# Kernel tuning notes

Measured on AMD Instinct MI355X. Metric: run time of the kernel, lower is better.

Reference implementation:

```python
import jax, jax.numpy as jnp
import numpy as np

L = 24
D = 2048
NUM_BLOCKS = 8
EPS = 1e-6
B, T = 2, 1024


def _block_layout(num_layers, num_blocks):
    base = num_layers // num_blocks
    rem = num_layers % num_blocks
    sizes = [base] * num_blocks
    if rem:
        sizes[-1] += rem
    starts = list(np.cumsum([0] + sizes[:-1]))
    return sizes, starts


def _rmsnorm(x, weight, eps=EPS):
    # x: (..., d)
    var = jnp.mean(x * x, axis=-1, keepdims=True)
    return x * jax.lax.rsqrt(var + eps) * weight


def setup_inputs() -> dict:
    key = jax.random.key(0)
    k1, k2, k3 = jax.random.split(key, 3)
    layer_outputs = jax.random.normal(k1, (L, B, T, D), dtype=jnp.float32)
    embedding = jax.random.normal(k2, (B, T, D), dtype=jnp.float32)
    queries = jax.random.normal(k3, (L, D), dtype=jnp.float32) * 0.02
    key_norm_weight = jnp.ones((D,), dtype=jnp.float32)
    return {
        "layer_outputs": layer_outputs,
        "embedding": embedding,
        "queries": queries,
        "key_norm_weight": key_norm_weight,
    }


def reference(layer_outputs, embedding, queries, key_norm_weight):
    """Faithful port of BlockAttnRes.compute_all_inputs.

    layer_outputs: (L, B, T, d)  -- f_l(h_l) for each layer
    embedding:     (B, T, d)     -- b_0
    queries:       (L, d)        -- zero-init pseudo-queries (randn here)
    key_norm_weight: (d,)        -- RMSNorm scale
    Returns (L, B, T, d): AttnRes input h_l for each layer.
    """
    num_layers = layer_outputs.shape[0]
    sizes, starts = _block_layout(num_layers, NUM_BLOCKS)

    block_reprs = [embedding]
    partial = None
    inputs = []
    block_n = 0
    for l in range(num_layers):  # fixed structural loop over layers
        # advance block index
        while l >= starts[block_n] + sizes[block_n]:
            block_n += 1
        i = l - starts[block_n]
        sources = list(block_reprs)
        if i > 0 and partial is not None:
            sources.append(partial)
        v_stack = jnp.stack(sources, axis=2)            # (B, T, n, d)
        k_stack = _rmsnorm(v_stack, key_norm_weight)    # (B, T, n, d)
        scores = jnp.einsum("btnd,d->btn", k_stack, queries[l])
        alpha = jax.nn.softmax(scores, axis=-1)         # (B, T, n)
        h = jnp.einsum("btn,btnd->btd", alpha, v_stack)
        inputs.append(h)
        f_l = layer_outputs[l]
        partial = f_l if partial is None else partial + f_l
        if i + 1 >= sizes[block_n]:
            block_reprs.append(partial)
            partial = None
    return jnp.stack(inputs, axis=0)  # (L, B, T, d)
```

## Files before the change

### kernel.cpp

```cpp
#include <hip/hip_runtime.h>
#include <hip/hip_bf16.h>

constexpr int LAYERS = 24;
constexpr int DIM    = 2048;
constexpr int NBLK   = 8;
constexpr float EPSV = 1e-6f;
constexpr int TPB    = 512;
constexpr int EPT    = 4;
constexpr int NSLOT  = 147;
constexpr int RSTR   = NSLOT + 2;

typedef float vf4 __attribute__((ext_vector_type(4)));

__device__ constexpr int OFF_TAB[24] =
    {0,1,4,7,10,14,18,22,27,32,37,43,49,55,62,69,76,84,92,100,109,118,127,137};
__device__ constexpr int SSQS[7] = {9,21,36,54,75,99,126};

__device__ __forceinline__ unsigned pk2(float a, float b) {
    __hip_bfloat162 h2(__float2bfloat16(a), __float2bfloat16(b));
    union { __hip_bfloat162 h; unsigned u; } c; c.h = h2; return c.u;
}
__device__ __forceinline__ float upk(unsigned p, int hi) {
    union { unsigned u; float f; } c;
    c.u = hi ? (p & 0xffff0000u) : (p << 16);
    return c.f;
}

template<int CTRL>
__device__ __forceinline__ float dpp_add(float x) {
    int y = __builtin_amdgcn_update_dpp(0, __float_as_int(x), CTRL, 0xF, 0xF, true);
    return x + __int_as_float(y);
}
__device__ __forceinline__ float grp16_sum(float x) {
    x = dpp_add<0xB1>(x);
    x = dpp_add<0x4E>(x);
    x = dpp_add<0x141>(x);
    x = dpp_add<0x140>(x);
    return x;
}

__global__ void prep_qw_kernel(const float* __restrict__ q,
                               const float* __restrict__ w,
                               float* __restrict__ qw, int n) {
    int idx = blockIdx.x * blockDim.x + threadIdx.x;
    if (idx < n) qw[idx] = q[idx] * w[idx & (DIM - 1)];
}

template<bool PREMUL>
__global__ void __launch_bounds__(TPB, 4)
block_attn_res_kernel(const float* __restrict__ lo,
                      const float* __restrict__ emb,
                      const float* __restrict__ q1,
                      const float* __restrict__ wgt,
                      float* __restrict__ out,
                      int bt_total)
{
    const int bt   = blockIdx.x;
    const int tid  = threadIdx.x;
    const int lane = tid & 63;
    const int wid  = tid >> 6;
    const int grp  = (wid << 2) | (lane >> 4);
    const int c0   = tid * 4;

    __shared__ float red[32][RSTR];
    __shared__ float redJ[NSLOT + 1];
    __shared__ float ab[LAYERS][12];

    const float invD = 1.f / (float)DIM;
    const size_t lstride = (size_t)bt_total * DIM;
    const float* lop = lo + (size_t)bt * DIM + c0;

    auto wred = [&](float x, int slot) {
        x = grp16_sum(x);
        if ((lane & 15) == 0) red[grp][slot] = x;
    };

    float wv[EPT];
    if (!PREMUL) {
        vf4 w0 = *reinterpret_cast<const vf4*>(wgt + c0);
        wv[0]=w0.x; wv[1]=w0.y; wv[2]=w0.z; wv[3]=w0.w;
    }

    float e[EPT];
    {
        vf4 v0 = __builtin_nontemporal_load(
            reinterpret_cast<const vf4*>(emb + (size_t)bt * DIM + c0));
        e[0]=v0.x; e[1]=v0.y; e[2]=v0.z; e[3]=v0.w;
    }

    unsigned pp[16][EPT/2];
    unsigned Spk[NBLK-1][EPT/2];
    float part[EPT];

    {
        vf4 u0 = __builtin_nontemporal_load(reinterpret_cast<const vf4*>(lop));
        part[0]=u0.x; part[1]=u0.y; part[2]=u0.z; part[3]=u0.w;

        vf4 w0; w0.x=e[0]; w0.y=e[1]; w0.z=e[2]; w0.w=e[3];
        *reinterpret_cast<vf4*>(out + (size_t)bt * DIM + c0) = w0;

        float sq = e[0]*e[0] + e[1]*e[1] + e[2]*e[2] + e[3]*e[3];
        wred(sq, 0);
    }

    float fb[8][EPT], qb[2][EPT];
    {
        #pragma unroll
        for (int k = 1; k <= 8; ++k) {
            vf4 u = __builtin_nontemporal_load(
                reinterpret_cast<const vf4*>(lop + (size_t)k * lstride));
            fb[k & 7][0]=u.x; fb[k & 7][1]=u.y; fb[k & 7][2]=u.z; fb[k & 7][3]=u.w;
        }
        vf4 q;
        q = *reinterpret_cast<const vf4*>(q1 + (size_t)1 * DIM + c0);
        qb[1][0]=q.x; qb[1][1]=q.y; qb[1][2]=q.z; qb[1][3]=q.w;
        q = *reinterpret_cast<const vf4*>(q1 + (size_t)2 * DIM + c0);
        qb[0][0]=q.x; qb[0][1]=q.y; qb[0][2]=q.z; qb[0][3]=q.w;
    }

    #pragma unroll
    for (int l = 1; l < LAYERS; ++l) {
        const int m   = l / 3;
        const int i   = l - 3 * m;
        const int off = OFF_TAB[l];
        const int pf  = l & 7;
        const int pq  = l & 1;

        float qwv[EPT];
        #pragma unroll
        for (int j = 0; j < EPT; ++j)
            qwv[j] = PREMUL ? qb[pq][j] : qb[pq][j] * wv[j];
        float fC[EPT];
        if (l < LAYERS - 1) {
            #pragma unroll
            for (int j = 0; j < EPT; ++j) fC[j] = fb[pf][j];
        }

        if (l + 8 <= LAYERS - 2) {
            vf4 u0 = __builtin_nontemporal_load(
                reinterpret_cast<const vf4*>(lop + (size_t)(l + 8) * lstride));
            fb[pf][0]=u0.x; fb[pf][1]=u0.y; fb[pf][2]=u0.z; fb[pf][3]=u0.w;
        }
        if (l + 2 <= LAYERS - 1) {
            vf4 v0 = *reinterpret_cast<const vf4*>(q1 + (size_t)(l + 2) * DIM + c0);
            qb[pq][0]=v0.x; qb[pq][1]=v0.y; qb[pq][2]=v0.z; qb[pq][3]=v0.w;
        }

        {
            float dv = e[0]*qwv[0] + e[1]*qwv[1] + e[2]*qwv[2] + e[3]*qwv[3];
            wred(dv, off);
        }
        #pragma unroll
        for (int s = 0; s < NBLK - 1; ++s) {
            if (s < m) {
                float dv;
                if (s == m - 1 && i == 0) {
                    dv = part[0]*qwv[0] + part[1]*qwv[1]
                       + part[2]*qwv[2] + part[3]*qwv[3];
                } else {
                    dv = upk(Spk[s][0],0)*qwv[0] + upk(Spk[s][0],1)*qwv[1]
                       + upk(Spk[s][1],0)*qwv[2] + upk(Spk[s][1],1)*qwv[3];
                }
                wred(dv, off + 1 + s);
            }
        }
        if (i > 0) {
            float dv = part[0]*qwv[0] + part[1]*qwv[1]
                     + part[2]*qwv[2] + part[3]*qwv[3];
            float sq = part[0]*part[0] + part[1]*part[1]
                     + part[2]*part[2] + part[3]*part[3];
            wred(dv, off + m + 1);
            wred(sq, off + m + 2);
            const int si = 2 * m + (i - 1);
            pp[si][0] = pk2(part[0], part[1]);
            pp[si][1] = pk2(part[2], part[3]);
        } else {
            float sq = part[0]*part[0] + part[1]*part[1]
                     + part[2]*part[2] + part[3]*part[3];
            wred(sq, off + m + 1);
        }

        if (l < LAYERS - 1) {
            if (i == 0) {
                #pragma unroll
                for (int j = 0; j < EPT; ++j) part[j] = fC[j];
            } else {
                #pragma unroll
                for (int j = 0; j < EPT; ++j) part[j] += fC[j];
            }
            if (i == 2 && m < NBLK - 1) {
                Spk[m][0] = pk2(part[0], part[1]);
                Spk[m][1] = pk2(part[2], part[3]);
            }
        }
    }

    __syncthreads();

    if (tid < NSLOT) {
        float s = 0.f;
        #pragma unroll
        for (int g = 0; g < 32; ++g) s += red[g][tid];
        redJ[tid] = s;
    }
    __syncthreads();

    if (tid >= 1 && tid < LAYERS) {
        const int l = tid;
        const int m = l / 3;
        const int i = l - 3 * m;
        const int off = OFF_TAB[l];
        const float ssqe = redJ[0];
        float sce = redJ[off] * rsqrtf(ssqe * invD + EPSV);
        float mx = sce;
        float scS[NBLK - 1];
        #pragma unroll
        for (int s = 0; s < NBLK - 1; ++s) {
            if (s < m) {
                scS[s] = redJ[off + 1 + s] * rsqrtf(redJ[SSQS[s]] * invD + EPSV);
                mx = fmaxf(mx, scS[s]);
            }
        }
        float scp = 0.f;
        if (i > 0) {
            scp = redJ[off + m + 1] * rsqrtf(redJ[off + m + 2] * invD + EPSV);
            mx = fmaxf(mx, scp);
        }
        float ee = __expf(sce - mx), den = ee;
        float es[NBLK - 1];
        #pragma unroll
        for (int s = 0; s < NBLK - 1; ++s) {
            es[s] = (s < m) ? __expf(scS[s] - mx) : 0.f;
            den += es[s];
        }
        float ep = 0.f;
        if (i > 0) { ep = __expf(scp - mx); den += ep; }
        const float inv = 1.f / den;
        ab[l][0] = ee * inv;
        #pragma unroll
        for (int s = 0; s < NBLK - 1; ++s)
            if (s < m) ab[l][1 + s] = es[s] * inv;
        if (i > 0) ab[l][1 + m] = ep * inv;
    }
    __syncthreads();

    #pragma unroll
    for (int l = 1; l < LAYERS; ++l) {
        const int m = l / 3;
        const int i = l - 3 * m;

        float h[EPT];
        {
            const float a0 = ab[l][0];
            #pragma unroll
            for (int j = 0; j < EPT; ++j) h[j] = a0 * e[j];
        }
        #pragma unroll
        for (int s = 0; s < NBLK - 1; ++s) {
            if (s < m) {
                const float a = ab[l][1 + s];
                h[0] += a * upk(Spk[s][0],0);
                h[1] += a * upk(Spk[s][0],1);
                h[2] += a * upk(Spk[s][1],0);
                h[3] += a * upk(Spk[s][1],1);
            }
        }
        if (i > 0) {
            const float a = ab[l][1 + m];
            const int si = 2 * m + (i - 1);
            h[0] += a * upk(pp[si][0],0);
            h[1] += a * upk(pp[si][0],1);
            h[2] += a * upk(pp[si][1],0);
            h[3] += a * upk(pp[si][1],1);
        }

        {
            vf4 w0; w0.x=h[0]; w0.y=h[1]; w0.z=h[2]; w0.w=h[3];
            *reinterpret_cast<vf4*>(out + ((size_t)l * bt_total + bt) * DIM + c0) = w0;
        }
    }
}

extern "C" void kernel_launch(void* const* d_in, const int* in_sizes, int n_in,
                              void* d_out, int out_size, void* d_ws, size_t ws_size,
                              hipStream_t stream) {
    const float* lo  = (const float*)d_in[0];
    const float* emb = (const float*)d_in[1];
    const float* qry = (const float*)d_in[2];
    const float* wgt = (const float*)d_in[3];
    float* outp = (float*)d_out;

    const int bt_total = in_sizes[1] / DIM;
    const int nq = in_sizes[2];

    if (ws_size >= (size_t)nq * sizeof(float)) {
        float* qwbuf = (float*)d_ws;
        prep_qw_kernel<<<(nq + 255) / 256, 256, 0, stream>>>(qry, wgt, qwbuf, nq);
        block_attn_res_kernel<true><<<bt_total, TPB, 0, stream>>>(
            lo, emb, qwbuf, nullptr, outp, bt_total);
    } else {
        block_attn_res_kernel<false><<<bt_total, TPB, 0, stream>>>(
            lo, emb, qry, wgt, outp, bt_total);
    }
}
```

Before: 195.6 us.

## Split layer pipeline in two halves to overlap output writes with loads

Splits the per-row computation into two phases. After the first 11 layers, the partial reductions and softmax for those layers are computed. Their outputs are then emitted, interleaved with the score accumulation for layers 12-23, so stores overlap the remaining loads. The prefetch depth for layer outputs drops from 8 to 4 slots, which frees registers. The cost is extra block-wide barriers and a shallower load pipeline.

```diff
diff --git a/kernel.cpp b/kernel.cpp
--- a/kernel.cpp
+++ b/kernel.cpp
@@ -8,6 +8,7 @@
 constexpr int TPB    = 512;
 constexpr int EPT    = 4;
 constexpr int NSLOT  = 147;
+constexpr int ASLOT  = 49;
 constexpr int RSTR   = NSLOT + 2;
 
 typedef float vf4 __attribute__((ext_vector_type(4)));
@@ -92,38 +93,43 @@
     unsigned Spk[NBLK-1][EPT/2];
     float part[EPT];
 
-    {
-        vf4 u0 = __builtin_nontemporal_load(reinterpret_cast<const vf4*>(lop));
-        part[0]=u0.x; part[1]=u0.y; part[2]=u0.z; part[3]=u0.w;
-
-        vf4 w0; w0.x=e[0]; w0.y=e[1]; w0.z=e[2]; w0.w=e[3];
-        *reinterpret_cast<vf4*>(out + (size_t)bt * DIM + c0) = w0;
-
-        float sq = e[0]*e[0] + e[1]*e[1] + e[2]*e[2] + e[3]*e[3];
-        wred(sq, 0);
-    }
-
-    float fb[8][EPT], qb[2][EPT];
-    {
-        #pragma unroll
-        for (int k = 1; k <= 8; ++k) {
-            vf4 u = __builtin_nontemporal_load(
-                reinterpret_cast<const vf4*>(lop + (size_t)k * lstride));
-            fb[k & 7][0]=u.x; fb[k & 7][1]=u.y; fb[k & 7][2]=u.z; fb[k & 7][3]=u.w;
-        }
-        vf4 q;
-        q = *reinterpret_cast<const vf4*>(q1 + (size_t)1 * DIM + c0);
-        qb[1][0]=q.x; qb[1][1]=q.y; qb[1][2]=q.z; qb[1][3]=q.w;
-        q = *reinterpret_cast<const vf4*>(q1 + (size_t)2 * DIM + c0);
-        qb[0][0]=q.x; qb[0][1]=q.y; qb[0][2]=q.z; qb[0][3]=q.w;
-    }
-
-    #pragma unroll
-    for (int l = 1; l < LAYERS; ++l) {
+    auto emit = [&](int l) {
+        const int m = l / 3;
+        const int i = l - 3 * m;
+        float h[EPT];
+        {
+            const float a0 = ab[l][0];
+            #pragma unroll
+            for (int j = 0; j < EPT; ++j) h[j] = a0 * e[j];
+        }
+        #pragma unroll
+        for (int s = 0; s < NBLK - 1; ++s) {
+            if (s < m) {
+                const float a = ab[l][1 + s];
+                h[0] += a * upk(Spk[s][0],0);
+                h[1] += a * upk(Spk[s][0],1);
+                h[2] += a * upk(Spk[s][1],0);
+                h[3] += a * upk(Spk[s][1],1);
+            }
+        }
+        if (i > 0) {
+            const float a = ab[l][1 + m];
+            const int si = 2 * m + (i - 1);
+            h[0] += a * upk(pp[si][0],0);
+            h[1] += a * upk(pp[si][0],1);
+            h[2] += a * upk(pp[si][1],0);
+            h[3] += a * upk(pp[si][1],1);
+        }
+        vf4 w0; w0.x=h[0]; w0.y=h[1]; w0.z=h[2]; w0.w=h[3];
+        *reinterpret_cast<vf4*>(out + ((size_t)l * bt_total + bt) * DIM + c0) = w0;
+    };
+
+    float fb[4][EPT], qb[2][EPT];
+    auto p1_body = [&](int l) {
         const int m   = l / 3;
         const int i   = l - 3 * m;
         const int off = OFF_TAB[l];
-        const int pf  = l & 7;
+        const int pf  = l & 3;
         const int pq  = l & 1;
 
         float qwv[EPT];
@@ -136,9 +142,9 @@
             for (int j = 0; j < EPT; ++j) fC[j] = fb[pf][j];
         }
 
-        if (l + 8 <= LAYERS - 2) {
+        if (l + 4 <= LAYERS - 2) {
             vf4 u0 = __builtin_nontemporal_load(
-                reinterpret_cast<const vf4*>(lop + (size_t)(l + 8) * lstride));
+                reinterpret_cast<const vf4*>(lop + (size_t)(l + 4) * lstride));
             fb[pf][0]=u0.x; fb[pf][1]=u0.y; fb[pf][2]=u0.z; fb[pf][3]=u0.w;
         }
         if (l + 2 <= LAYERS - 1) {
@@ -193,20 +199,9 @@
                 Spk[m][1] = pk2(part[2], part[3]);
             }
         }
-    }
-
-    __syncthreads();
-
-    if (tid < NSLOT) {
-        float s = 0.f;
-        #pragma unroll
-        for (int g = 0; g < 32; ++g) s += red[g][tid];
-        redJ[tid] = s;
-    }
-    __syncthreads();
-
-    if (tid >= 1 && tid < LAYERS) {
-        const int l = tid;
+    };
+
+    auto softmax_l = [&](int l) {
         const int m = l / 3;
         const int i = l - 3 * m;
         const int off = OFF_TAB[l];
@@ -241,44 +236,65 @@
         for (int s = 0; s < NBLK - 1; ++s)
             if (s < m) ab[l][1 + s] = es[s] * inv;
         if (i > 0) ab[l][1 + m] = ep * inv;
-    }
-    __syncthreads();
-
+    };
+
+    {
+        vf4 u0 = __builtin_nontemporal_load(reinterpret_cast<const vf4*>(lop));
+        part[0]=u0.x; part[1]=u0.y; part[2]=u0.z; part[3]=u0.w;
+
+        vf4 w0; w0.x=e[0]; w0.y=e[1]; w0.z=e[2]; w0.w=e[3];
+        *reinterpret_cast<vf4*>(out + (size_t)bt * DIM + c0) = w0;
+
+        float sq = e[0]*e[0] + e[1]*e[1] + e[2]*e[2] + e[3]*e[3];
+        wred(sq, 0);
+    }
+    {
+        #pragma unroll
+        for (int k = 1; k <= 4; ++k) {
+            vf4 u = __builtin_nontemporal_load(
+                reinterpret_cast<const vf4*>(lop + (size_t)k * lstride));
+            fb[k & 3][0]=u.x; fb[k & 3][1]=u.y; fb[k & 3][2]=u.z; fb[k & 3][3]=u.w;
+        }
+        vf4 q;
+        q = *reinterpret_cast<const vf4*>(q1 + (size_t)1 * DIM + c0);
+        qb[1][0]=q.x; qb[1][1]=q.y; qb[1][2]=q.z; qb[1][3]=q.w;
+        q = *reinterpret_cast<const vf4*>(q1 + (size_t)2 * DIM + c0);
+        qb[0][0]=q.x; qb[0][1]=q.y; qb[0][2]=q.z; qb[0][3]=q.w;
+    }
     #pragma unroll
-    for (int l = 1; l < LAYERS; ++l) {
-        const int m = l / 3;
-        const int i = l - 3 * m;
-
-        float h[EPT];
-        {
-            const float a0 = ab[l][0];
-            #pragma unroll
-            for (int j = 0; j < EPT; ++j) h[j] = a0 * e[j];
-        }
-        #pragma unroll
-        for (int s = 0; s < NBLK - 1; ++s) {
-            if (s < m) {
-                const float a = ab[l][1 + s];
-                h[0] += a * upk(Spk[s][0],0);
-                h[1] += a * upk(Spk[s][0],1);
-                h[2] += a * upk(Spk[s][1],0);
-                h[3] += a * upk(Spk[s][1],1);
-            }
-        }
-        if (i > 0) {
-            const float a = ab[l][1 + m];
-            const int si = 2 * m + (i - 1);
-            h[0] += a * upk(pp[si][0],0);
-            h[1] += a * upk(pp[si][0],1);
-            h[2] += a * upk(pp[si][1],0);
-            h[3] += a * upk(pp[si][1],1);
-        }
-
-        {
-            vf4 w0; w0.x=h[0]; w0.y=h[1]; w0.z=h[2]; w0.w=h[3];
-            *reinterpret_cast<vf4*>(out + ((size_t)l * bt_total + bt) * DIM + c0) = w0;
-        }
-    }
+    for (int l = 1; l <= 11; ++l) p1_body(l);
+
+    __syncthreads();
+    if (tid < ASLOT) {
+        float s = 0.f;
+        #pragma unroll
+        for (int g = 0; g < 32; ++g) s += red[g][tid];
+        redJ[tid] = s;
+    }
+    __syncthreads();
+    if (tid >= 1 && tid <= 11) softmax_l(tid);
+    __syncthreads();
+
+    #pragma unroll
+    for (int l = 12; l < LAYERS; ++l) {
+        p1_body(l);
+        if (l <= 22) emit(l - 11);
+    }
+
+    __syncthreads();
+    if (tid < NSLOT - ASLOT) {
+        const int slot = ASLOT + tid;
+        float s = 0.f;
+        #pragma unroll
+        for (int g = 0; g < 32; ++g) s += red[g][slot];
+        redJ[slot] = s;
+    }
+    __syncthreads();
+    if (tid >= 12 && tid < LAYERS) softmax_l(tid);
+    __syncthreads();
+
+    #pragma unroll
+    for (int l = 12; l < LAYERS; ++l) emit(l);
 }
 
 extern "C" void kernel_launch(void* const* d_in, const int* in_sizes, int n_in,
```

Result: faster. 179.1 us (-8.5%).
